# Kernel optimization log

Hardware: AMD Instinct MI355X
Metric: run time of the kernel (lower is better)

Reference implementation:

```python
import jax, jax.numpy as jnp
import numpy as np

B, L, D = 2, 8192, 1024


def setup_inputs() -> dict:
    key = jax.random.key(0)
    ks = jax.random.split(key, 6)
    x = jax.random.normal(ks[0], (B, L, D), dtype=jnp.float32)
    # phazor param init (torch): exp(2j*pi*arange(D)/D) * |randn(D)|
    mag = jnp.abs(jax.random.normal(ks[1], (D,), dtype=jnp.float32))
    ang = (2.0 * np.pi * jnp.arange(D) / D).astype(jnp.float32)
    phazor_real = mag * jnp.cos(ang)
    phazor_imag = mag * jnp.sin(ang)
    # phazor_init ~ complex randn
    phazor_init_real = jax.random.normal(ks[2], (D,), dtype=jnp.float32)
    phazor_init_imag = jax.random.normal(ks[3], (D,), dtype=jnp.float32)
    # last_conv_init ~ complex randn (first-call hidden state, broadcast over batch)
    last_conv_real = jax.random.normal(ks[4], (D,), dtype=jnp.float32)
    last_conv_imag = jax.random.normal(ks[5], (D,), dtype=jnp.float32)
    return {
        "x": x,
        "phazor_real": phazor_real, "phazor_imag": phazor_imag,
        "phazor_init_real": phazor_init_real, "phazor_init_imag": phazor_init_imag,
        "last_conv_real": last_conv_real, "last_conv_imag": last_conv_imag,
    }


def reference(x, phazor_real, phazor_imag, phazor_init_real, phazor_init_imag,
              last_conv_real, last_conv_imag):
    b, length, dim = x.shape
    dtype = x.dtype
    # reparameterized decay: magnitude exp(-|p|^2), keep angle of p
    ph = jnp.exp(-(phazor_real * phazor_real + phazor_imag * phazor_imag)) \
         * jnp.exp(1j * jnp.arctan2(phazor_imag, phazor_real))          # [D] complex
    # phazor_progression[t, d] = ph[d] ** t
    prog = jnp.power(ph[None, :], jnp.arange(length)[:, None])           # [L, D]
    pinit = phazor_init_real + 1j * phazor_init_imag                     # [D]
    filt = prog * pinit[None, :]                                         # [L, D]
    # FFT convolution with zero-padding to 2L (linear convolution)
    filt_fft = jnp.fft.fft(filt, n=2 * length, axis=0)                   # [2L, D]
    x_fft = jnp.fft.fft(x.astype(jnp.complex64), n=2 * length, axis=1)   # [B, 2L, D]
    conv = jnp.fft.ifft(filt_fft[None, :, :] * x_fft, axis=1)[:, :length, :]  # [B, L, D]
    # carry in hidden state from previous chunk (here: learned init, broadcast over batch)
    last = (last_conv_real + 1j * last_conv_imag)[None, None, :]          # [1, 1, D]
    conv_with_past = conv + last * prog[None, :, :] * ph[None, None, :]
    return conv_with_past.real.astype(dtype)
```

## Files before the change

### kernel.cpp

```cpp
#include <hip/hip_runtime.h>

#define BB 2
#define LL 8192
#define DD 1024
#define NC 128
#define TT 64
#define NPAIR (DD/2)
#define FOLD_BATCH 16

__device__ __forceinline__ void compute_ph(float pr, float pi, float& phr, float& phi) {
    float r2 = fmaf(pr, pr, pi * pi);
    float mag = expf(-r2);
    float r = sqrtf(r2);
    if (r > 1e-30f) {
        float inv = mag / r;
        phr = pr * inv;
        phi = pi * inv;
    } else {
        phr = mag;
        phi = 0.0f;
    }
}

__global__ __launch_bounds__(256) void k_partial(
    const float* __restrict__ x,
    const float* __restrict__ pr, const float* __restrict__ pi,
    const float* __restrict__ qr, const float* __restrict__ qi,
    float4* __restrict__ partial)
{
    const int p = blockIdx.x * 256 + threadIdx.x;
    const int j = blockIdx.y;
    const int b = blockIdx.z;
    const int d0 = 2 * p, d1 = d0 + 1;

    float phr0, phi0, phr1, phi1;
    compute_ph(pr[d0], pi[d0], phr0, phi0);
    compute_ph(pr[d1], pi[d1], phr1, phi1);
    const float q0r = qr[d0], q0i = qi[d0], q1r = qr[d1], q1i = qi[d1];

    const float2* xp = (const float2*)(x + ((size_t)b * LL + (size_t)j * TT) * DD) + p;

    float sr0 = 0.f, si0 = 0.f, sr1 = 0.f, si1 = 0.f;
    #pragma unroll 16
    for (int t = 0; t < TT; ++t) {
        float2 xv = xp[(size_t)t * NPAIR];
        float nr0 = fmaf(phr0, sr0, fmaf(-phi0, si0, q0r * xv.x));
        float ni0 = fmaf(phi0, sr0, fmaf(phr0, si0, q0i * xv.x));
        float nr1 = fmaf(phr1, sr1, fmaf(-phi1, si1, q1r * xv.y));
        float ni1 = fmaf(phi1, sr1, fmaf(phr1, si1, q1i * xv.y));
        sr0 = nr0; si0 = ni0; sr1 = nr1; si1 = ni1;
    }
    partial[((size_t)b * NC + j) * NPAIR + p] = make_float4(sr0, si0, sr1, si1);
}

__global__ __launch_bounds__(256) void k_final(
    const float* __restrict__ x,
    const float* __restrict__ pr, const float* __restrict__ pi,
    const float* __restrict__ qr, const float* __restrict__ qi,
    const float* __restrict__ lr, const float* __restrict__ li,
    const float4* __restrict__ partial,
    float* __restrict__ out)
{
    const int p = blockIdx.x * 256 + threadIdx.x;
    const int j = blockIdx.y;
    const int b = blockIdx.z;
    const int d0 = 2 * p, d1 = d0 + 1;

    float phr0, phi0, phr1, phi1;
    compute_ph(pr[d0], pi[d0], phr0, phi0);
    compute_ph(pr[d1], pi[d1], phr1, phi1);
    const float q0r = qr[d0], q0i = qi[d0], q1r = qr[d1], q1i = qi[d1];

    float a0r = phr0, a0i = phi0, a1r = phr1, a1i = phi1;
    #pragma unroll
    for (int k = 0; k < 6; ++k) {
        float n0r = a0r * a0r - a0i * a0i, n0i = 2.f * a0r * a0i;
        float n1r = a1r * a1r - a1i * a1i, n1i = 2.f * a1r * a1i;
        a0r = n0r; a0i = n0i; a1r = n1r; a1i = n1i;
    }

    float S0r = lr[d0], S0i = li[d0], S1r = lr[d1], S1i = li[d1];
    const float4* pb = partial + (size_t)b * NC * NPAIR + p;
    for (int bs = 0; bs < j; bs += FOLD_BATCH) {
        float4 buf[FOLD_BATCH];
        #pragma unroll
        for (int u = 0; u < FOLD_BATCH; ++u) {
            int k = bs + u;
            int kc = (k < j) ? k : (j - 1);
            buf[u] = pb[(size_t)kc * NPAIR];
        }
        #pragma unroll
        for (int u = 0; u < FOLD_BATCH; ++u) {
            int k = bs + u;
            if (k < j) {
                float n0r = fmaf(a0r, S0r, fmaf(-a0i, S0i, buf[u].x));
                float n0i = fmaf(a0i, S0r, fmaf(a0r, S0i, buf[u].y));
                float n1r = fmaf(a1r, S1r, fmaf(-a1i, S1i, buf[u].z));
                float n1i = fmaf(a1i, S1r, fmaf(a1r, S1i, buf[u].w));
                S0r = n0r; S0i = n0i; S1r = n1r; S1i = n1i;
            }
        }
    }

    const size_t rowbase = (size_t)b * LL + (size_t)j * TT;
    const float2* xp = (const float2*)(x + rowbase * DD) + p;
    float2* op = (float2*)(out + rowbase * DD) + p;
    #pragma unroll 16
    for (int t = 0; t < TT; ++t) {
        float2 xv = xp[(size_t)t * NPAIR];
        float n0r = fmaf(phr0, S0r, fmaf(-phi0, S0i, q0r * xv.x));
        float n0i = fmaf(phi0, S0r, fmaf(phr0, S0i, q0i * xv.x));
        float n1r = fmaf(phr1, S1r, fmaf(-phi1, S1i, q1r * xv.y));
        float n1i = fmaf(phi1, S1r, fmaf(phr1, S1i, q1i * xv.y));
        S0r = n0r; S0i = n0i; S1r = n1r; S1i = n1i;
        op[(size_t)t * NPAIR] = make_float2(n0r, n1r);
    }
}

extern "C" void kernel_launch(void* const* d_in, const int* in_sizes, int n_in,
                              void* d_out, int out_size, void* d_ws, size_t ws_size,
                              hipStream_t stream) {
    const float* x  = (const float*)d_in[0];
    const float* pr = (const float*)d_in[1];
    const float* pi = (const float*)d_in[2];
    const float* qr = (const float*)d_in[3];
    const float* qi = (const float*)d_in[4];
    const float* lr = (const float*)d_in[5];
    const float* li = (const float*)d_in[6];
    float* out = (float*)d_out;

    float4* partial = (float4*)d_ws;

    dim3 grid(NPAIR / 256, NC, BB);
    k_partial<<<grid, 256, 0, stream>>>(x, pr, pi, qr, qi, partial);
    k_final<<<grid, 256, 0, stream>>>(x, pr, pi, qr, qi, lr, li, partial, out);
}
```

Before: 43.93 us.

## Precompute chunk carry states in a separate scan kernel instead of per-block refolding

Adds a k_scan kernel that sequentially folds the per-chunk partial sums once per channel pair and stores each chunk's incoming state to workspace. k_final then just loads its state rather than redundantly folding all preceding partials, removing quadratic fold work and load imbalance. It also batches k_final's x loads and output stores into 32-element register arrays and raises the unroll in k_partial. The trade-off is an extra launch and a scan kernel with very few blocks running a long serial dependency chain.

Result: slower. 52.76 us (+20.1%).

```diff
diff --git a/kernel.cpp b/kernel.cpp
--- a/kernel.cpp
+++ b/kernel.cpp
@@ -6,7 +6,6 @@
 #define NC 128
 #define TT 64
 #define NPAIR (DD/2)
-#define FOLD_BATCH 16
 
 __device__ __forceinline__ void compute_ph(float pr, float pi, float& phr, float& phi) {
     float r2 = fmaf(pr, pr, pi * pi);
@@ -41,7 +40,7 @@
     const float2* xp = (const float2*)(x + ((size_t)b * LL + (size_t)j * TT) * DD) + p;
 
     float sr0 = 0.f, si0 = 0.f, sr1 = 0.f, si1 = 0.f;
-    #pragma unroll 16
+    #pragma unroll 32
     for (int t = 0; t < TT; ++t) {
         float2 xv = xp[(size_t)t * NPAIR];
         float nr0 = fmaf(phr0, sr0, fmaf(-phi0, si0, q0r * xv.x));
@@ -53,12 +52,68 @@
     partial[((size_t)b * NC + j) * NPAIR + p] = make_float4(sr0, si0, sr1, si1);
 }
 
+#define SD 8
+__global__ __launch_bounds__(256) void k_scan(
+    const float* __restrict__ pr, const float* __restrict__ pi,
+    const float* __restrict__ lr, const float* __restrict__ li,
+    const float4* __restrict__ partial,
+    float4* __restrict__ Sarr)
+{
+    const int idx = blockIdx.x * 256 + threadIdx.x;
+    const int p = idx & (NPAIR - 1);
+    const int b = idx >> 9;
+    const int d0 = 2 * p, d1 = d0 + 1;
+
+    float phr0, phi0, phr1, phi1;
+    compute_ph(pr[d0], pi[d0], phr0, phi0);
+    compute_ph(pr[d1], pi[d1], phr1, phi1);
+
+    float a0r = phr0, a0i = phi0, a1r = phr1, a1i = phi1;
+    #pragma unroll
+    for (int k = 0; k < 6; ++k) {
+        float n0r = a0r * a0r - a0i * a0i, n0i = 2.f * a0r * a0i;
+        float n1r = a1r * a1r - a1i * a1i, n1i = 2.f * a1r * a1i;
+        a0r = n0r; a0i = n0i; a1r = n1r; a1i = n1i;
+    }
+
+    float S0r = lr[d0], S0i = li[d0], S1r = lr[d1], S1i = li[d1];
+    const float4* pb = partial + (size_t)b * NC * NPAIR + p;
+    float4* sb = Sarr + (size_t)b * NC * NPAIR + p;
+
+    float4 buf[SD];
+    #pragma unroll
+    for (int u = 0; u < SD; ++u) buf[u] = pb[(size_t)u * NPAIR];
+
+    #pragma unroll
+    for (int r = 0; r < NC / SD; ++r) {
+        float4 nxt[SD];
+        if (r < NC / SD - 1) {
+            #pragma unroll
+            for (int u = 0; u < SD; ++u)
+                nxt[u] = pb[(size_t)((r + 1) * SD + u) * NPAIR];
+        }
+        #pragma unroll
+        for (int u = 0; u < SD; ++u) {
+            int j = r * SD + u;
+            sb[(size_t)j * NPAIR] = make_float4(S0r, S0i, S1r, S1i);
+            float n0r = fmaf(a0r, S0r, fmaf(-a0i, S0i, buf[u].x));
+            float n0i = fmaf(a0i, S0r, fmaf(a0r, S0i, buf[u].y));
+            float n1r = fmaf(a1r, S1r, fmaf(-a1i, S1i, buf[u].z));
+            float n1i = fmaf(a1i, S1r, fmaf(a1r, S1i, buf[u].w));
+            S0r = n0r; S0i = n0i; S1r = n1r; S1i = n1i;
+        }
+        if (r < NC / SD - 1) {
+            #pragma unroll
+            for (int u = 0; u < SD; ++u) buf[u] = nxt[u];
+        }
+    }
+}
+
 __global__ __launch_bounds__(256) void k_final(
     const float* __restrict__ x,
     const float* __restrict__ pr, const float* __restrict__ pi,
     const float* __restrict__ qr, const float* __restrict__ qi,
-    const float* __restrict__ lr, const float* __restrict__ li,
-    const float4* __restrict__ partial,
+    const float4* __restrict__ Sarr,
     float* __restrict__ out)
 {
     const int p = blockIdx.x * 256 + threadIdx.x;
@@ -71,49 +126,32 @@
     compute_ph(pr[d1], pi[d1], phr1, phi1);
     const float q0r = qr[d0], q0i = qi[d0], q1r = qr[d1], q1i = qi[d1];
 
-    float a0r = phr0, a0i = phi0, a1r = phr1, a1i = phi1;
-    #pragma unroll
-    for (int k = 0; k < 6; ++k) {
-        float n0r = a0r * a0r - a0i * a0i, n0i = 2.f * a0r * a0i;
-        float n1r = a1r * a1r - a1i * a1i, n1i = 2.f * a1r * a1i;
-        a0r = n0r; a0i = n0i; a1r = n1r; a1i = n1i;
-    }
-
-    float S0r = lr[d0], S0i = li[d0], S1r = lr[d1], S1i = li[d1];
-    const float4* pb = partial + (size_t)b * NC * NPAIR + p;
-    for (int bs = 0; bs < j; bs += FOLD_BATCH) {
-        float4 buf[FOLD_BATCH];
-        #pragma unroll
-        for (int u = 0; u < FOLD_BATCH; ++u) {
-            int k = bs + u;
-            int kc = (k < j) ? k : (j - 1);
-            buf[u] = pb[(size_t)kc * NPAIR];
-        }
-        #pragma unroll
-        for (int u = 0; u < FOLD_BATCH; ++u) {
-            int k = bs + u;
-            if (k < j) {
-                float n0r = fmaf(a0r, S0r, fmaf(-a0i, S0i, buf[u].x));
-                float n0i = fmaf(a0i, S0r, fmaf(a0r, S0i, buf[u].y));
-                float n1r = fmaf(a1r, S1r, fmaf(-a1i, S1i, buf[u].z));
-                float n1i = fmaf(a1i, S1r, fmaf(a1r, S1i, buf[u].w));
-                S0r = n0r; S0i = n0i; S1r = n1r; S1i = n1i;
-            }
-        }
-    }
+    float4 S = Sarr[((size_t)b * NC + j) * NPAIR + p];
+    float S0r = S.x, S0i = S.y, S1r = S.z, S1i = S.w;
 
     const size_t rowbase = (size_t)b * LL + (size_t)j * TT;
     const float2* xp = (const float2*)(x + rowbase * DD) + p;
     float2* op = (float2*)(out + rowbase * DD) + p;
-    #pragma unroll 16
-    for (int t = 0; t < TT; ++t) {
-        float2 xv = xp[(size_t)t * NPAIR];
-        float n0r = fmaf(phr0, S0r, fmaf(-phi0, S0i, q0r * xv.x));
-        float n0i = fmaf(phi0, S0r, fmaf(phr0, S0i, q0i * xv.x));
-        float n1r = fmaf(phr1, S1r, fmaf(-phi1, S1i, q1r * xv.y));
-        float n1i = fmaf(phi1, S1r, fmaf(phr1, S1i, q1i * xv.y));
-        S0r = n0r; S0i = n0i; S1r = n1r; S1i = n1i;
-        op[(size_t)t * NPAIR] = make_float2(n0r, n1r);
+
+    #pragma unroll
+    for (int half = 0; half < 2; ++half) {
+        float2 xv[32];
+        #pragma unroll
+        for (int u = 0; u < 32; ++u)
+            xv[u] = xp[(size_t)(half * 32 + u) * NPAIR];
+        float2 ov[32];
+        #pragma unroll
+        for (int u = 0; u < 32; ++u) {
+            float n0r = fmaf(phr0, S0r, fmaf(-phi0, S0i, q0r * xv[u].x));
+            float n0i = fmaf(phi0, S0r, fmaf(phr0, S0i, q0i * xv[u].x));
+            float n1r = fmaf(phr1, S1r, fmaf(-phi1, S1i, q1r * xv[u].y));
+            float n1i = fmaf(phi1, S1r, fmaf(phr1, S1i, q1i * xv[u].y));
+            S0r = n0r; S0i = n0i; S1r = n1r; S1i = n1i;
+            ov[u] = make_float2(n0r, n1r);
+        }
+        #pragma unroll
+        for (int u = 0; u < 32; ++u)
+            op[(size_t)(half * 32 + u) * NPAIR] = ov[u];
     }
 }
 
@@ -130,8 +168,10 @@
     float* out = (float*)d_out;
 
     float4* partial = (float4*)d_ws;
+    float4* Sarr    = partial + (size_t)BB * NC * NPAIR;
 
     dim3 grid(NPAIR / 256, NC, BB);
     k_partial<<<grid, 256, 0, stream>>>(x, pr, pi, qr, qi, partial);
-    k_final<<<grid, 256, 0, stream>>>(x, pr, pi, qr, qi, lr, li, partial, out);
+    k_scan<<<(BB * NPAIR) / 256, 256, 0, stream>>>(pr, pi, lr, li, partial, Sarr);
+    k_final<<<grid, 256, 0, stream>>>(x, pr, pi, qr, qi, Sarr, out);
 }
```

## Fuse partial and final scan kernels with inter-block flag synchronization

Applied to the files above, without the earlier changes.

Merges the chunk-partial kernel and the final fold/output kernel into one launch. Each block writes its chunk partial, publishes a release flag, then spins on the flags of earlier chunks in its column before folding and emitting output. This removes the second kernel launch and lets the re-read of x overlap with other blocks' work. In exchange it adds a memset of the flag area, spin-waiting, and reliance on blocks being co-resident or dispatched in order.

Result: slower. 133.7 us (+204.4%).

```diff
diff --git a/kernel.cpp b/kernel.cpp
--- a/kernel.cpp
+++ b/kernel.cpp
@@ -6,6 +6,7 @@
 #define NC 128
 #define TT 64
 #define NPAIR (DD/2)
+#define NCOL (NPAIR/256)
 #define FOLD_BATCH 16
 
 __device__ __forceinline__ void compute_ph(float pr, float pi, float& phr, float& phi) {
@@ -22,54 +23,58 @@
     }
 }
 
-__global__ __launch_bounds__(256) void k_partial(
+__global__ __launch_bounds__(256, 4) void k_fused(
     const float* __restrict__ x,
     const float* __restrict__ pr, const float* __restrict__ pi,
     const float* __restrict__ qr, const float* __restrict__ qi,
-    float4* __restrict__ partial)
+    const float* __restrict__ lr, const float* __restrict__ li,
+    float4* __restrict__ partial,
+    unsigned int* __restrict__ flags,
+    float* __restrict__ out)
 {
-    const int p = blockIdx.x * 256 + threadIdx.x;
-    const int j = blockIdx.y;
-    const int b = blockIdx.z;
-    const int d0 = 2 * p, d1 = d0 + 1;
+    const int tid = threadIdx.x;
+    const int p   = blockIdx.x * 256 + tid;
+    const int j   = blockIdx.y;
+    const int b   = blockIdx.z;
+    const int d0  = 2 * p, d1 = d0 + 1;
+    unsigned int* colflags = flags + ((size_t)b * NCOL + blockIdx.x) * NC;
 
     float phr0, phi0, phr1, phi1;
     compute_ph(pr[d0], pi[d0], phr0, phi0);
     compute_ph(pr[d1], pi[d1], phr1, phi1);
     const float q0r = qr[d0], q0i = qi[d0], q1r = qr[d1], q1i = qi[d1];
 
-    const float2* xp = (const float2*)(x + ((size_t)b * LL + (size_t)j * TT) * DD) + p;
+    const size_t rowbase = (size_t)b * LL + (size_t)j * TT;
+    const float2* xp = (const float2*)(x + rowbase * DD) + p;
 
-    float sr0 = 0.f, si0 = 0.f, sr1 = 0.f, si1 = 0.f;
-    #pragma unroll 16
-    for (int t = 0; t < TT; ++t) {
-        float2 xv = xp[(size_t)t * NPAIR];
-        float nr0 = fmaf(phr0, sr0, fmaf(-phi0, si0, q0r * xv.x));
-        float ni0 = fmaf(phi0, sr0, fmaf(phr0, si0, q0i * xv.x));
-        float nr1 = fmaf(phr1, sr1, fmaf(-phi1, si1, q1r * xv.y));
-        float ni1 = fmaf(phi1, sr1, fmaf(phr1, si1, q1i * xv.y));
-        sr0 = nr0; si0 = ni0; sr1 = nr1; si1 = ni1;
+    {
+        float sr0 = 0.f, si0 = 0.f, sr1 = 0.f, si1 = 0.f;
+        #pragma unroll 32
+        for (int t = 0; t < TT; ++t) {
+            float2 xv = xp[(size_t)t * NPAIR];
+            float nr0 = fmaf(phr0, sr0, fmaf(-phi0, si0, q0r * xv.x));
+            float ni0 = fmaf(phi0, sr0, fmaf(phr0, si0, q0i * xv.x));
+            float nr1 = fmaf(phr1, sr1, fmaf(-phi1, si1, q1r * xv.y));
+            float ni1 = fmaf(phi1, sr1, fmaf(phr1, si1, q1i * xv.y));
+            sr0 = nr0; si0 = ni0; sr1 = nr1; si1 = ni1;
+        }
+        partial[((size_t)b * NC + j) * NPAIR + p] = make_float4(sr0, si0, sr1, si1);
     }
-    partial[((size_t)b * NC + j) * NPAIR + p] = make_float4(sr0, si0, sr1, si1);
-}
 
-__global__ __launch_bounds__(256) void k_final(
-    const float* __restrict__ x,
-    const float* __restrict__ pr, const float* __restrict__ pi,
-    const float* __restrict__ qr, const float* __restrict__ qi,
-    const float* __restrict__ lr, const float* __restrict__ li,
-    const float4* __restrict__ partial,
-    float* __restrict__ out)
-{
-    const int p = blockIdx.x * 256 + threadIdx.x;
-    const int j = blockIdx.y;
-    const int b = blockIdx.z;
-    const int d0 = 2 * p, d1 = d0 + 1;
+    __syncthreads();
+    if (tid == 0) {
+        __threadfence();
+        __hip_atomic_store(&colflags[j], 1u, __ATOMIC_RELEASE, __HIP_MEMORY_SCOPE_AGENT);
+    }
 
-    float phr0, phi0, phr1, phi1;
-    compute_ph(pr[d0], pi[d0], phr0, phi0);
-    compute_ph(pr[d1], pi[d1], phr1, phi1);
-    const float q0r = qr[d0], q0i = qi[d0], q1r = qr[d1], q1i = qi[d1];
+    if (tid < j) {
+        while (__hip_atomic_load(&colflags[tid], __ATOMIC_ACQUIRE,
+                                 __HIP_MEMORY_SCOPE_AGENT) == 0u) {
+            __builtin_amdgcn_s_sleep(2);
+        }
+    }
+    __syncthreads();
+    __threadfence();
 
     float a0r = phr0, a0i = phi0, a1r = phr1, a1i = phi1;
     #pragma unroll
@@ -102,8 +107,6 @@
         }
     }
 
-    const size_t rowbase = (size_t)b * LL + (size_t)j * TT;
-    const float2* xp = (const float2*)(x + rowbase * DD) + p;
     float2* op = (float2*)(out + rowbase * DD) + p;
     #pragma unroll 16
     for (int t = 0; t < TT; ++t) {
@@ -129,9 +132,11 @@
     const float* li = (const float*)d_in[6];
     float* out = (float*)d_out;
 
-    float4* partial = (float4*)d_ws;
+    unsigned int* flags = (unsigned int*)d_ws;
+    float4* partial = (float4*)((char*)d_ws + 8192);
 
-    dim3 grid(NPAIR / 256, NC, BB);
-    k_partial<<<grid, 256, 0, stream>>>(x, pr, pi, qr, qi, partial);
-    k_final<<<grid, 256, 0, stream>>>(x, pr, pi, qr, qi, lr, li, partial, out);
+    hipMemsetAsync(d_ws, 0, 8192, stream);
+
+    dim3 grid(NCOL, NC, BB);
+    k_fused<<<grid, 256, 0, stream>>>(x, pr, pi, qr, qi, lr, li, partial, flags, out);
 }
```

## Halve chunk length and double-buffer x loads in the scan kernels

Applied to the files above, without the earlier changes.

Doubles the number of time chunks (NC 128→256, TT 64→32) for more parallelism, and updates the chunk-decay power from ph^64 to ph^32 to match. The per-thread time loops become explicit double-buffered batches of 8 loads, so loads for the next batch are issued while the current batch's recurrence runs. In exchange the serial fold over prior chunk partials in k_final gets twice as long, and the partial workspace doubles.

Result: slower. 61.57 us (+40.1%).

```diff
diff --git a/kernel.cpp b/kernel.cpp
--- a/kernel.cpp
+++ b/kernel.cpp
@@ -3,8 +3,8 @@
 #define BB 2
 #define LL 8192
 #define DD 1024
-#define NC 128
-#define TT 64
+#define NC 256
+#define TT 32
 #define NPAIR (DD/2)
 #define FOLD_BATCH 16
 
@@ -21,6 +21,25 @@
         phi = 0.0f;
     }
 }
+
+
+#define LD8(buf, g) \
+    { _Pragma("unroll") for (int u = 0; u < 8; ++u) \
+        buf[u] = xp[(size_t)((g) * 8 + u) * NPAIR]; }
+
+#define CP8(buf) \
+    { _Pragma("unroll") for (int u = 0; u < 8; ++u) { \
+        float2 xv = buf[u]; \
+        float nr0 = fmaf(phr0, s0r, fmaf(-phi0, s0i, q0r * xv.x)); \
+        float ni0 = fmaf(phi0, s0r, fmaf( phr0, s0i, q0i * xv.x)); \
+        float nr1 = fmaf(phr1, s1r, fmaf(-phi1, s1i, q1r * xv.y)); \
+        float ni1 = fmaf(phi1, s1r, fmaf( phr1, s1i, q1i * xv.y)); \
+        s0r = nr0; s0i = ni0; s1r = nr1; s1i = ni1; \
+        buf[u] = make_float2(nr0, nr1); } }
+
+#define ST8(buf, g) \
+    { _Pragma("unroll") for (int u = 0; u < 8; ++u) \
+        op[(size_t)((g) * 8 + u) * NPAIR] = buf[u]; }
 
 __global__ __launch_bounds__(256) void k_partial(
     const float* __restrict__ x,
@@ -40,17 +59,15 @@
 
     const float2* xp = (const float2*)(x + ((size_t)b * LL + (size_t)j * TT) * DD) + p;
 
-    float sr0 = 0.f, si0 = 0.f, sr1 = 0.f, si1 = 0.f;
-    #pragma unroll 16
-    for (int t = 0; t < TT; ++t) {
-        float2 xv = xp[(size_t)t * NPAIR];
-        float nr0 = fmaf(phr0, sr0, fmaf(-phi0, si0, q0r * xv.x));
-        float ni0 = fmaf(phi0, sr0, fmaf(phr0, si0, q0i * xv.x));
-        float nr1 = fmaf(phr1, sr1, fmaf(-phi1, si1, q1r * xv.y));
-        float ni1 = fmaf(phi1, sr1, fmaf(phr1, si1, q1i * xv.y));
-        sr0 = nr0; si0 = ni0; sr1 = nr1; si1 = ni1;
-    }
-    partial[((size_t)b * NC + j) * NPAIR + p] = make_float4(sr0, si0, sr1, si1);
+    float s0r = 0.f, s0i = 0.f, s1r = 0.f, s1i = 0.f;
+    float2 bufA[8], bufB[8];
+    LD8(bufA, 0); LD8(bufB, 1);
+    CP8(bufA);    LD8(bufA, 2);
+    CP8(bufB);    LD8(bufB, 3);
+    CP8(bufA);
+    CP8(bufB);
+
+    partial[((size_t)b * NC + j) * NPAIR + p] = make_float4(s0r, s0i, s1r, s1i);
 }
 
 __global__ __launch_bounds__(256) void k_final(
@@ -73,13 +90,13 @@
 
     float a0r = phr0, a0i = phi0, a1r = phr1, a1i = phi1;
     #pragma unroll
-    for (int k = 0; k < 6; ++k) {
+    for (int k = 0; k < 5; ++k) {
         float n0r = a0r * a0r - a0i * a0i, n0i = 2.f * a0r * a0i;
         float n1r = a1r * a1r - a1i * a1i, n1i = 2.f * a1r * a1i;
         a0r = n0r; a0i = n0i; a1r = n1r; a1i = n1i;
     }
 
-    float S0r = lr[d0], S0i = li[d0], S1r = lr[d1], S1i = li[d1];
+    float s0r = lr[d0], s0i = li[d0], s1r = lr[d1], s1i = li[d1];
     const float4* pb = partial + (size_t)b * NC * NPAIR + p;
     for (int bs = 0; bs < j; bs += FOLD_BATCH) {
         float4 buf[FOLD_BATCH];
@@ -93,11 +110,11 @@
         for (int u = 0; u < FOLD_BATCH; ++u) {
             int k = bs + u;
             if (k < j) {
-                float n0r = fmaf(a0r, S0r, fmaf(-a0i, S0i, buf[u].x));
-                float n0i = fmaf(a0i, S0r, fmaf(a0r, S0i, buf[u].y));
-                float n1r = fmaf(a1r, S1r, fmaf(-a1i, S1i, buf[u].z));
-                float n1i = fmaf(a1i, S1r, fmaf(a1r, S1i, buf[u].w));
-                S0r = n0r; S0i = n0i; S1r = n1r; S1i = n1i;
+                float n0r = fmaf(a0r, s0r, fmaf(-a0i, s0i, buf[u].x));
+                float n0i = fmaf(a0i, s0r, fmaf( a0r, s0i, buf[u].y));
+                float n1r = fmaf(a1r, s1r, fmaf(-a1i, s1i, buf[u].z));
+                float n1i = fmaf(a1i, s1r, fmaf( a1r, s1i, buf[u].w));
+                s0r = n0r; s0i = n0i; s1r = n1r; s1i = n1i;
             }
         }
     }
@@ -105,16 +122,13 @@
     const size_t rowbase = (size_t)b * LL + (size_t)j * TT;
     const float2* xp = (const float2*)(x + rowbase * DD) + p;
     float2* op = (float2*)(out + rowbase * DD) + p;
-    #pragma unroll 16
-    for (int t = 0; t < TT; ++t) {
-        float2 xv = xp[(size_t)t * NPAIR];
-        float n0r = fmaf(phr0, S0r, fmaf(-phi0, S0i, q0r * xv.x));
-        float n0i = fmaf(phi0, S0r, fmaf(phr0, S0i, q0i * xv.x));
-        float n1r = fmaf(phr1, S1r, fmaf(-phi1, S1i, q1r * xv.y));
-        float n1i = fmaf(phi1, S1r, fmaf(phr1, S1i, q1i * xv.y));
-        S0r = n0r; S0i = n0i; S1r = n1r; S1i = n1i;
-        op[(size_t)t * NPAIR] = make_float2(n0r, n1r);
-    }
+
+    float2 bufA[8], bufB[8];
+    LD8(bufA, 0); LD8(bufB, 1);
+    CP8(bufA);    ST8(bufA, 0); LD8(bufA, 2);
+    CP8(bufB);    ST8(bufB, 1); LD8(bufB, 3);
+    CP8(bufA);    ST8(bufA, 2);
+    CP8(bufB);    ST8(bufB, 3);
 }
 
 extern "C" void kernel_launch(void* const* d_in, const int* in_sizes, int n_in,
```
